# Kernel optimization log

Hardware: AMD Instinct MI355X
Metric: run time of the kernel (lower is better)

Reference implementation:

```python
import jax, jax.numpy as jnp
import numpy as np

N, NODES, DIN, HID, M, OUT_FE = 8192, 20000, 768, 256, 4096, 50


def setup_inputs() -> dict:
    key = jax.random.key(0)
    ks = jax.random.split(key, 12)
    s = 0.02  # small init scale to keep tanh in its linear-ish range
    return {
        "t": jax.random.normal(ks[0], (N, DIN), jnp.float32),
        "AGE_inx": jax.random.normal(ks[1], (NODES, DIN), jnp.float32),
        "Endx": jax.random.randint(ks[2], (M,), 0, NODES, jnp.int32),
        "W_age": jax.random.normal(ks[3], (DIN, DIN), jnp.float32) * s,
        "b_age": jnp.zeros((DIN,), jnp.float32),
        "W_prjT": jax.random.normal(ks[4], (HID, DIN), jnp.float32) * s,
        "b_prjT": jnp.zeros((HID,), jnp.float32),
        "W_prjL": jax.random.normal(ks[5], (HID, DIN), jnp.float32) * s,
        "b_prjL": jnp.zeros((HID,), jnp.float32),
        "outW": jax.random.normal(ks[6], (M, HID), jnp.float32) * s,
        "outb": jax.random.normal(ks[7], (M,), jnp.float32) * s,
        "W_fc3": jax.random.normal(ks[8], (OUT_FE, HID), jnp.float32) * s,
        "b_fc3": jnp.zeros((OUT_FE,), jnp.float32),
    }


def _lintrans(x, W, b):
    # AGE LinTrans: Linear -> per-row min-max scale -> L2 normalize
    z = x @ W.T + b                                   # [NODES, 768]
    zmin = jnp.min(z, axis=1, keepdims=True)
    zmax = jnp.max(z, axis=1, keepdims=True)
    z = (z - zmin) / (zmax - zmin)
    norm = jnp.sqrt(jnp.sum(z * z, axis=1, keepdims=True))
    return z / jnp.maximum(norm, 1e-12)


def reference(t, AGE_inx, Endx, W_age, b_age, W_prjT, b_prjT,
              W_prjL, b_prjL, outW, outb, W_fc3, b_fc3):
    AGE_E = _lintrans(AGE_inx, W_age, b_age)          # [NODES, 768]
    h = jnp.tanh(t @ W_prjT.T + b_prjT)               # [N, 256]
    E = jnp.tanh(AGE_E[Endx] @ W_prjL.T + b_prjL)     # [M, 256]
    # sum_d h[n,d]*E[m,d]*outW[m,d] == h @ (E*outW).T  (avoids [N,M,256] blowup)
    o_c = h @ (E * outW).T + outb                     # [N, M]
    o_f = h @ W_fc3.T + b_fc3                         # [N, OUT_FE]
    return (o_c, o_f)
```

## Files before the change

kernel.cpp:

```cpp
#include <hip/hip_runtime.h>
#include <hip/hip_bf16.h>
#include <cstdint>
#include <cstddef>

typedef __hip_bfloat16 bf16;
typedef __attribute__((ext_vector_type(4))) float f32x4;
typedef __attribute__((ext_vector_type(8))) short s16x8;

__device__ __forceinline__ void gload_lds16(const void* g, void* l) {
    __builtin_amdgcn_global_load_lds(
        (const __attribute__((address_space(1))) unsigned int*)g,
        (__attribute__((address_space(3))) unsigned int*)l,
        16, 0, 0);
}

__device__ __forceinline__ short f2bs(float x) {
    bf16 h = __float2bfloat16(x);
    return *reinterpret_cast<short*>(&h);
}

__device__ __forceinline__ s16x8 pack8(f32x4 u, f32x4 v) {
    s16x8 p;
    p[0] = f2bs(u[0]); p[1] = f2bs(u[1]); p[2] = f2bs(u[2]); p[3] = f2bs(u[3]);
    p[4] = f2bs(v[0]); p[5] = f2bs(v[1]); p[6] = f2bs(v[2]); p[7] = f2bs(v[3]);
    return p;
}

template<int TANH, int MULW, int F32OUT, int NGUARD, int ASRC, int BSRC>
__device__ __forceinline__ void gemm_body(
    short* __restrict__ sAB,
    int bm, int bn,
    const void* __restrict__ Aptr, const void* __restrict__ Bptr,
    const int* __restrict__ gidx,
    const float* __restrict__ bias, const float* __restrict__ Mul,
    void* __restrict__ Cout, int M, int N, int K, int ldc)
{
    short* sA = sAB;
    short* sB = sAB + 128 * 64;

    const int tid  = threadIdx.x;
    const int lane = tid & 63;
    const int wave = tid >> 6;
    const int wr = wave >> 1, wc = wave & 1;
    const int l15 = lane & 15, quad = lane >> 4;

    int    slot[4];
    size_t a_off[4], b_off[4];
#pragma unroll
    for (int j = 0; j < 4; ++j) {
        int S   = (wave * 4 + j) * 64 + lane;
        int row = S >> 3;
        int cc  = (S & 7) ^ (row & 7);
        slot[j] = S * 8;
        if (ASRC == 2)
            a_off[j] = (size_t)gidx[bm * 128 + row] * K + cc * 8;
        else
            a_off[j] = (size_t)(bm * 128 + row) * K + cc * 8;
        int ng = bn * 128 + row;
        if (NGUARD) ng = (ng < N) ? ng : (N - 1);
        b_off[j] = (size_t)ng * K + cc * 8;
    }

    f32x4 acc[4][4];
#pragma unroll
    for (int i = 0; i < 4; ++i)
#pragma unroll
        for (int j = 0; j < 4; ++j)
            acc[i][j] = (f32x4){0.f, 0.f, 0.f, 0.f};

    f32x4 pa0[4], pa1[4], pb0[4], pb1[4];
    if (ASRC != 0) {
#pragma unroll
        for (int j = 0; j < 4; ++j) {
            const float* s = (const float*)Aptr + a_off[j];
            pa0[j] = *(const f32x4*)s;
            pa1[j] = *(const f32x4*)(s + 4);
        }
    }
    if (BSRC != 0) {
#pragma unroll
        for (int j = 0; j < 4; ++j) {
            const float* s = (const float*)Bptr + b_off[j];
            pb0[j] = *(const f32x4*)s;
            pb1[j] = *(const f32x4*)(s + 4);
        }
    }

    for (int kt = 0; kt < K; kt += 64) {
#pragma unroll
        for (int j = 0; j < 4; ++j) {
            if (ASRC == 0)
                gload_lds16((const bf16*)Aptr + a_off[j] + kt, &sA[slot[j]]);
            else
                *(s16x8*)&sA[slot[j]] = pack8(pa0[j], pa1[j]);
        }
#pragma unroll
        for (int j = 0; j < 4; ++j) {
            if (BSRC == 0)
                gload_lds16((const bf16*)Bptr + b_off[j] + kt, &sB[slot[j]]);
            else
                *(s16x8*)&sB[slot[j]] = pack8(pb0[j], pb1[j]);
        }
        if (ASRC == 0 || BSRC == 0)
            asm volatile("s_waitcnt vmcnt(0)" ::: "memory");
        __syncthreads();

        if (kt + 64 < K) {
            if (ASRC != 0) {
#pragma unroll
                for (int j = 0; j < 4; ++j) {
                    const float* s = (const float*)Aptr + a_off[j] + kt + 64;
                    pa0[j] = *(const f32x4*)s;
                    pa1[j] = *(const f32x4*)(s + 4);
                }
            }
            if (BSRC != 0) {
#pragma unroll
                for (int j = 0; j < 4; ++j) {
                    const float* s = (const float*)Bptr + b_off[j] + kt + 64;
                    pb0[j] = *(const f32x4*)s;
                    pb1[j] = *(const f32x4*)(s + 4);
                }
            }
        }

#pragma unroll
        for (int ks = 0; ks < 2; ++ks) {
            s16x8 afr[4], bfr[4];
#pragma unroll
            for (int i = 0; i < 4; ++i) {
                int r = wr * 64 + i * 16 + l15;
                int q = ks * 4 + quad;
                afr[i] = *(const s16x8*)&sA[(r * 8 + (q ^ (r & 7))) * 8];
            }
#pragma unroll
            for (int j = 0; j < 4; ++j) {
                int r = wc * 64 + j * 16 + l15;
                int q = ks * 4 + quad;
                bfr[j] = *(const s16x8*)&sB[(r * 8 + (q ^ (r & 7))) * 8];
            }
#pragma unroll
            for (int i = 0; i < 4; ++i)
#pragma unroll
                for (int j = 0; j < 4; ++j)
                    acc[i][j] = __builtin_amdgcn_mfma_f32_16x16x32_bf16(
                        afr[i], bfr[j], acc[i][j], 0, 0, 0);
        }
        __syncthreads();
    }

    if (NGUARD) {
#pragma unroll
        for (int j = 0; j < 4; ++j) {
            int colg = bn * 128 + wc * 64 + j * 16 + l15;
            if (colg >= N) continue;
            float bv = bias[colg];
#pragma unroll
            for (int i = 0; i < 4; ++i) {
                int row0 = bm * 128 + wr * 64 + i * 16 + quad * 4;
#pragma unroll
                for (int r = 0; r < 4; ++r) {
                    float v = acc[i][j][r] + bv;
                    if (TANH) v = tanhf(v);
                    if (MULW) v *= Mul[(size_t)(row0 + r) * N + colg];
                    if (F32OUT)
                        ((float*)Cout)[(size_t)(row0 + r) * ldc + colg] = v;
                    else
                        ((bf16*)Cout)[(size_t)(row0 + r) * ldc + colg] = __float2bfloat16(v);
                }
            }
        }
        return;
    }

    float* wt = (float*)sAB + wave * 2048;
#pragma unroll
    for (int half = 0; half < 2; ++half) {
#pragma unroll
        for (int jj = 0; jj < 2; ++jj) {
            int j = half * 2 + jj;
            int colg = bn * 128 + wc * 64 + j * 16 + l15;
            float bv = bias[colg];
#pragma unroll
            for (int i = 0; i < 4; ++i) {
                int row0 = bm * 128 + wr * 64 + i * 16 + quad * 4;
#pragma unroll
                for (int r = 0; r < 4; ++r) {
                    float v = acc[i][j][r] + bv;
                    if (TANH) v = tanhf(v);
                    if (MULW) v *= Mul[(size_t)(row0 + r) * N + colg];
                    int lrow = i * 16 + quad * 4 + r;
                    int lcol = jj * 16 + l15;
                    wt[lrow * 32 + (lcol ^ ((lrow & 7) << 2))] = v;
                }
            }
        }
        __syncthreads();
        if (F32OUT) {
            int r8 = lane >> 3, seg = lane & 7;
#pragma unroll
            for (int ii = 0; ii < 8; ++ii) {
                int lrow = ii * 8 + r8;
                f32x4 v = *(const f32x4*)&wt[lrow * 32 + ((seg * 4) ^ ((lrow & 7) << 2))];
                size_t ro = (size_t)(bm * 128 + wr * 64 + lrow) * ldc
                          + bn * 128 + wc * 64 + half * 32 + seg * 4;
                *(f32x4*)&((float*)Cout)[ro] = v;
            }
        } else {
            int r4 = lane >> 2, sg = lane & 3;
#pragma unroll
            for (int ii = 0; ii < 4; ++ii) {
                int lrow = ii * 16 + r4;
                int c0 = sg * 8;
                f32x4 u = *(const f32x4*)&wt[lrow * 32 + ((c0    ) ^ ((lrow & 7) << 2))];
                f32x4 w = *(const f32x4*)&wt[lrow * 32 + ((c0 + 4) ^ ((lrow & 7) << 2))];
                s16x8 p = pack8(u, w);
                size_t ro = (size_t)(bm * 128 + wr * 64 + lrow) * ldc
                          + bn * 128 + wc * 64 + half * 32 + c0;
                *(s16x8*)&((bf16*)Cout)[ro] = p;
            }
        }
        __syncthreads();
    }
}

__global__ __launch_bounds__(256)
void mm_z(const float* __restrict__ AGEinx, const int* __restrict__ Endx,
          const float* __restrict__ W_age, const float* __restrict__ b_age,
          float* __restrict__ z)
{
    __shared__ short sAB[2 * 128 * 64];
    int b = blockIdx.x;
    gemm_body<0, 0, 1, 0, 2, 1>(sAB, b / 6, b % 6,
                                AGEinx, W_age, Endx, b_age, nullptr,
                                z, 4096, 768, 768, 768);
}

__global__ __launch_bounds__(256)
void mm_he2(const float* __restrict__ t, const float* __restrict__ W_prjT,
            const float* __restrict__ b_prjT, bf16* __restrict__ h,
            const bf16* __restrict__ AGE_E, const float* __restrict__ W_prjL,
            const float* __restrict__ b_prjL, const float* __restrict__ outW,
            bf16* __restrict__ E2)
{
    __shared__ short sAB[2 * 128 * 64];
    int b = blockIdx.x;
    if (b < 128) {
        gemm_body<1, 0, 0, 0, 1, 1>(sAB, b / 2, b % 2,
                                    t, W_prjT, nullptr, b_prjT, nullptr,
                                    h, 8192, 256, 768, 256);
    } else {
        int b2 = b - 128;
        gemm_body<1, 1, 0, 0, 0, 1>(sAB, b2 / 2, b2 % 2,
                                    AGE_E, W_prjL, nullptr, b_prjL, outW,
                                    E2, 4096, 256, 768, 256);
    }
}

__global__ __launch_bounds__(256)
void mm_out(const bf16* __restrict__ h, const bf16* __restrict__ E2,
            const float* __restrict__ outb, float* __restrict__ o_c,
            const float* __restrict__ W_fc3, const float* __restrict__ b_fc3,
            float* __restrict__ o_f)
{
    __shared__ short sAB[2 * 128 * 64];
    int b = blockIdx.x;
    if (b < 2048) {
        int bs = (b & 7) * 256 + (b >> 3);
        gemm_body<0, 0, 1, 0, 0, 0>(sAB, bs / 32, bs % 32,
                                    h, E2, nullptr, outb, nullptr,
                                    o_c, 8192, 4096, 256, 4096);
    } else {
        int b2 = b - 2048;
        gemm_body<0, 0, 1, 1, 0, 1>(sAB, b2, 0,
                                    h, W_fc3, nullptr, b_fc3, nullptr,
                                    o_f, 8192, 50, 256, 50);
    }
}

__global__ __launch_bounds__(256)
void lintrans_k(const float* __restrict__ z, bf16* __restrict__ out)
{
    __shared__ float rmin[4], rmax[4], rsum[4];
    const int row  = blockIdx.x;
    const int tid  = threadIdx.x;
    const int lane = tid & 63;
    const int wave = tid >> 6;
    const float* zr = z + (size_t)row * 768;

    float v0 = zr[tid], v1 = zr[tid + 256], v2 = zr[tid + 512];
    float mn = fminf(fminf(v0, v1), v2);
    float mx = fmaxf(fmaxf(v0, v1), v2);
#pragma unroll
    for (int o = 32; o > 0; o >>= 1) {
        mn = fminf(mn, __shfl_down(mn, o));
        mx = fmaxf(mx, __shfl_down(mx, o));
    }
    if (lane == 0) { rmin[wave] = mn; rmax[wave] = mx; }
    __syncthreads();
    float bmn = fminf(fminf(rmin[0], rmin[1]), fminf(rmin[2], rmin[3]));
    float bmx = fmaxf(fmaxf(rmax[0], rmax[1]), fmaxf(rmax[2], rmax[3]));
    float sc  = 1.f / (bmx - bmn);
    v0 = (v0 - bmn) * sc; v1 = (v1 - bmn) * sc; v2 = (v2 - bmn) * sc;
    float s = v0 * v0 + v1 * v1 + v2 * v2;
#pragma unroll
    for (int o = 32; o > 0; o >>= 1) s += __shfl_down(s, o);
    if (lane == 0) rsum[wave] = s;
    __syncthreads();
    float tot = rsum[0] + rsum[1] + rsum[2] + rsum[3];
    float inv = 1.f / fmaxf(sqrtf(tot), 1e-12f);
    out[(size_t)row * 768 + tid]       = __float2bfloat16(v0 * inv);
    out[(size_t)row * 768 + tid + 256] = __float2bfloat16(v1 * inv);
    out[(size_t)row * 768 + tid + 512] = __float2bfloat16(v2 * inv);
}

extern "C" void kernel_launch(void* const* d_in, const int* in_sizes, int n_in,
                              void* d_out, int out_size, void* d_ws, size_t ws_size,
                              hipStream_t stream)
{
    (void)in_sizes; (void)n_in; (void)out_size; (void)ws_size;

    const float* t_in   = (const float*)d_in[0];
    const float* AGEinx = (const float*)d_in[1];
    const int*   Endx   = (const int*)  d_in[2];
    const float* W_age  = (const float*)d_in[3];
    const float* b_age  = (const float*)d_in[4];
    const float* W_prjT = (const float*)d_in[5];
    const float* b_prjT = (const float*)d_in[6];
    const float* W_prjL = (const float*)d_in[7];
    const float* b_prjL = (const float*)d_in[8];
    const float* outW   = (const float*)d_in[9];
    const float* outb   = (const float*)d_in[10];
    const float* W_fc3  = (const float*)d_in[11];
    const float* b_fc3  = (const float*)d_in[12];

    char* ws = (char*)d_ws;
    size_t off = 0;
    float* z     = (float*)(ws + off);
    bf16*  h     = (bf16*) (ws + off); off += (size_t)4096 * 768 * 4;
    bf16*  AGE_E = (bf16*) (ws + off); off += (size_t)4096 * 768 * 2;
    bf16*  E2    = (bf16*) (ws + off); off += (size_t)4096 * 256 * 2;

    float* o_c = (float*)d_out;
    float* o_f = o_c + (size_t)8192 * 4096;

    mm_z<<<192, 256, 0, stream>>>(AGEinx, Endx, W_age, b_age, z);
    lintrans_k<<<4096, 256, 0, stream>>>(z, AGE_E);
    mm_he2<<<192, 256, 0, stream>>>(t_in, W_prjT, b_prjT, h,
                                    AGE_E, W_prjL, b_prjL, outW, E2);
    mm_out<<<2112, 256, 0, stream>>>(h, E2, outb, o_c, W_fc3, b_fc3, o_f);
}
```

Measured before the change: 300.8 us.

## Rebalance kernel grouping and use nontemporal stores for fp32 outputs

Moves the h projection GEMM into the first launch alongside the z GEMM, so 320 blocks fill the GPU instead of 192. The o_f GEMM moves into the E2 launch, leaving the big o_c GEMM as a clean kernel without the tail blocks. Fp32 outputs of the final GEMMs now use nontemporal stores to avoid polluting caches with the 128MB o_c write. The workspace is separated so h no longer aliases z, which costs extra workspace memory.

```diff
diff --git a/kernel.cpp b/kernel.cpp
--- a/kernel.cpp
+++ b/kernel.cpp
@@ -26,7 +26,7 @@
     return p;
 }
 
-template<int TANH, int MULW, int F32OUT, int NGUARD, int ASRC, int BSRC>
+template<int TANH, int MULW, int F32OUT, int NGUARD, int ASRC, int BSRC, int NT>
 __device__ __forceinline__ void gemm_body(
     short* __restrict__ sAB,
     int bm, int bn,
@@ -163,10 +163,13 @@
                     float v = acc[i][j][r] + bv;
                     if (TANH) v = tanhf(v);
                     if (MULW) v *= Mul[(size_t)(row0 + r) * N + colg];
-                    if (F32OUT)
-                        ((float*)Cout)[(size_t)(row0 + r) * ldc + colg] = v;
-                    else
+                    if (F32OUT) {
+                        float* p = &((float*)Cout)[(size_t)(row0 + r) * ldc + colg];
+                        if (NT) __builtin_nontemporal_store(v, p);
+                        else    *p = v;
+                    } else {
                         ((bf16*)Cout)[(size_t)(row0 + r) * ldc + colg] = __float2bfloat16(v);
+                    }
                 }
             }
         }
@@ -204,7 +207,8 @@
                 f32x4 v = *(const f32x4*)&wt[lrow * 32 + ((seg * 4) ^ ((lrow & 7) << 2))];
                 size_t ro = (size_t)(bm * 128 + wr * 64 + lrow) * ldc
                           + bn * 128 + wc * 64 + half * 32 + seg * 4;
-                *(f32x4*)&((float*)Cout)[ro] = v;
+                if (NT) __builtin_nontemporal_store(v, (f32x4*)&((float*)Cout)[ro]);
+                else    *(f32x4*)&((float*)Cout)[ro] = v;
             }
         } else {
             int r4 = lane >> 2, sg = lane & 3;
@@ -225,57 +229,57 @@
 }
 
 __global__ __launch_bounds__(256)
-void mm_z(const float* __restrict__ AGEinx, const int* __restrict__ Endx,
-          const float* __restrict__ W_age, const float* __restrict__ b_age,
-          float* __restrict__ z)
+void mm_zh(const float* __restrict__ AGEinx, const int* __restrict__ Endx,
+           const float* __restrict__ W_age, const float* __restrict__ b_age,
+           float* __restrict__ z,
+           const float* __restrict__ t, const float* __restrict__ W_prjT,
+           const float* __restrict__ b_prjT, bf16* __restrict__ h)
 {
     __shared__ short sAB[2 * 128 * 64];
     int b = blockIdx.x;
-    gemm_body<0, 0, 1, 0, 2, 1>(sAB, b / 6, b % 6,
-                                AGEinx, W_age, Endx, b_age, nullptr,
-                                z, 4096, 768, 768, 768);
+    if (b < 192) {
+        gemm_body<0, 0, 1, 0, 2, 1, 0>(sAB, b / 6, b % 6,
+                                       AGEinx, W_age, Endx, b_age, nullptr,
+                                       z, 4096, 768, 768, 768);
+    } else {
+        int b2 = b - 192;
+        gemm_body<1, 0, 0, 0, 1, 1, 0>(sAB, b2 / 2, b2 % 2,
+                                       t, W_prjT, nullptr, b_prjT, nullptr,
+                                       h, 8192, 256, 768, 256);
+    }
 }
 
 __global__ __launch_bounds__(256)
-void mm_he2(const float* __restrict__ t, const float* __restrict__ W_prjT,
-            const float* __restrict__ b_prjT, bf16* __restrict__ h,
-            const bf16* __restrict__ AGE_E, const float* __restrict__ W_prjL,
-            const float* __restrict__ b_prjL, const float* __restrict__ outW,
-            bf16* __restrict__ E2)
+void mm_e2of(const bf16* __restrict__ AGE_E, const float* __restrict__ W_prjL,
+             const float* __restrict__ b_prjL, const float* __restrict__ outW,
+             bf16* __restrict__ E2,
+             const bf16* __restrict__ h, const float* __restrict__ W_fc3,
+             const float* __restrict__ b_fc3, float* __restrict__ o_f)
 {
     __shared__ short sAB[2 * 128 * 64];
     int b = blockIdx.x;
-    if (b < 128) {
-        gemm_body<1, 0, 0, 0, 1, 1>(sAB, b / 2, b % 2,
-                                    t, W_prjT, nullptr, b_prjT, nullptr,
-                                    h, 8192, 256, 768, 256);
+    if (b < 64) {
+        gemm_body<1, 1, 0, 0, 0, 1, 0>(sAB, b / 2, b % 2,
+                                       AGE_E, W_prjL, nullptr, b_prjL, outW,
+                                       E2, 4096, 256, 768, 256);
     } else {
-        int b2 = b - 128;
-        gemm_body<1, 1, 0, 0, 0, 1>(sAB, b2 / 2, b2 % 2,
-                                    AGE_E, W_prjL, nullptr, b_prjL, outW,
-                                    E2, 4096, 256, 768, 256);
+        int b2 = b - 64;
+        gemm_body<0, 0, 1, 1, 0, 1, 1>(sAB, b2, 0,
+                                       h, W_fc3, nullptr, b_fc3, nullptr,
+                                       o_f, 8192, 50, 256, 50);
     }
 }
 
 __global__ __launch_bounds__(256)
-void mm_out(const bf16* __restrict__ h, const bf16* __restrict__ E2,
-            const float* __restrict__ outb, float* __restrict__ o_c,
-            const float* __restrict__ W_fc3, const float* __restrict__ b_fc3,
-            float* __restrict__ o_f)
+void mm_oc(const bf16* __restrict__ h, const bf16* __restrict__ E2,
+           const float* __restrict__ outb, float* __restrict__ o_c)
 {
     __shared__ short sAB[2 * 128 * 64];
     int b = blockIdx.x;
-    if (b < 2048) {
-        int bs = (b & 7) * 256 + (b >> 3);
-        gemm_body<0, 0, 1, 0, 0, 0>(sAB, bs / 32, bs % 32,
-                                    h, E2, nullptr, outb, nullptr,
-                                    o_c, 8192, 4096, 256, 4096);
-    } else {
-        int b2 = b - 2048;
-        gemm_body<0, 0, 1, 1, 0, 1>(sAB, b2, 0,
-                                    h, W_fc3, nullptr, b_fc3, nullptr,
-                                    o_f, 8192, 50, 256, 50);
-    }
+    int bs = (b & 7) * 256 + (b >> 3);
+    gemm_body<0, 0, 1, 0, 0, 0, 1>(sAB, bs / 32, bs % 32,
+                                   h, E2, nullptr, outb, nullptr,
+                                   o_c, 8192, 4096, 256, 4096);
 }
 
 __global__ __launch_bounds__(256)
@@ -336,17 +340,18 @@
 
     char* ws = (char*)d_ws;
     size_t off = 0;
-    float* z     = (float*)(ws + off);
-    bf16*  h     = (bf16*) (ws + off); off += (size_t)4096 * 768 * 4;
+    float* z     = (float*)(ws + off); off += (size_t)4096 * 768 * 4;
+    bf16*  h     = (bf16*) (ws + off); off += (size_t)8192 * 256 * 2;
     bf16*  AGE_E = (bf16*) (ws + off); off += (size_t)4096 * 768 * 2;
     bf16*  E2    = (bf16*) (ws + off); off += (size_t)4096 * 256 * 2;
 
     float* o_c = (float*)d_out;
     float* o_f = o_c + (size_t)8192 * 4096;
 
-    mm_z<<<192, 256, 0, stream>>>(AGEinx, Endx, W_age, b_age, z);
+    mm_zh<<<320, 256, 0, stream>>>(AGEinx, Endx, W_age, b_age, z,
+                                   t_in, W_prjT, b_prjT, h);
     lintrans_k<<<4096, 256, 0, stream>>>(z, AGE_E);
-    mm_he2<<<192, 256, 0, stream>>>(t_in, W_prjT, b_prjT, h,
-                                    AGE_E, W_prjL, b_prjL, outW, E2);
-    mm_out<<<2112, 256, 0, stream>>>(h, E2, outb, o_c, W_fc3, b_fc3, o_f);
-}
+    mm_e2of<<<128, 256, 0, stream>>>(AGE_E, W_prjL, b_prjL, outW, E2,
+                                     h, W_fc3, b_fc3, o_f);
+    mm_oc<<<2048, 256, 0, stream>>>(h, E2, outb, o_c);
+}
```

Result: no change. 306.4 us (+1.9%).
